# Kernel optimization log

Measured on AMD Instinct MI355X. Metric: run time of the kernel, lower is better.

The kernel has to match this reference:

```python
import jax, jax.numpy as jnp
import numpy as np

L, B, N, D, H = 2, 4, 2048, 1024, 16
DH = D // H
HID = 4 * D
EPS = 1e-5


def setup_inputs() -> dict:
    key = jax.random.key(0)
    ks = jax.random.split(key, 8)
    s = 0.02
    return {
        "tokens": jax.random.normal(ks[0], (B, N, D), jnp.float32),
        "ln1_g": jnp.ones((L, D), jnp.float32),
        "ln1_b": jnp.zeros((L, D), jnp.float32),
        "qkv_w": jax.random.normal(ks[1], (L, 3 * D, D), jnp.float32) * s,
        "qkv_b": jnp.zeros((L, 3 * D), jnp.float32),
        "out_w": jax.random.normal(ks[2], (L, D, D), jnp.float32) * s,
        "out_b": jnp.zeros((L, D), jnp.float32),
        "ln2_g": jnp.ones((L, D), jnp.float32),
        "ln2_b": jnp.zeros((L, D), jnp.float32),
        "fc1_w": jax.random.normal(ks[3], (L, HID, D), jnp.float32) * s,
        "fc1_b": jnp.zeros((L, HID), jnp.float32),
        "fc2_w": jax.random.normal(ks[4], (L, D, HID), jnp.float32) * s,
        "fc2_b": jnp.zeros((L, D), jnp.float32),
    }


def _layernorm(x, g, b):
    mu = jnp.mean(x, axis=-1, keepdims=True)
    var = jnp.mean(jnp.square(x - mu), axis=-1, keepdims=True)
    return (x - mu) * jax.lax.rsqrt(var + EPS) * g + b


def _mha(x, qkv_w, qkv_b, out_w, out_b):
    # nn.MultiheadAttention self-attention, batch_first=True
    qkv = x @ qkv_w.T + qkv_b                        # [B,N,3D]
    q, k, v = jnp.split(qkv, 3, axis=-1)
    q = q.reshape(B, N, H, DH)
    k = k.reshape(B, N, H, DH)
    v = v.reshape(B, N, H, DH)
    scores = jnp.einsum("bqhd,bkhd->bhqk", q, k) / np.sqrt(DH).astype(np.float32)
    attn = jax.nn.softmax(scores, axis=-1)
    o = jnp.einsum("bhqk,bkhd->bqhd", attn, v).reshape(B, N, D)
    return o @ out_w.T + out_b


def reference(tokens, ln1_g, ln1_b, qkv_w, qkv_b, out_w, out_b,
              ln2_g, ln2_b, fc1_w, fc1_b, fc2_w, fc2_b):
    x = tokens
    for i in range(L):
        # NOTE: the original reassigns tokens = norm1(tokens) before residual,
        # so the residual is taken on the NORMED tokens (faithful to source).
        x = _layernorm(x, ln1_g[i], ln1_b[i])
        x = x + _mha(x, qkv_w[i], qkv_b[i], out_w[i], out_b[i])
        x = _layernorm(x, ln2_g[i], ln2_b[i])
        h = jax.nn.gelu(x @ fc1_w[i].T + fc1_b[i], approximate=False)
        x = x + (h @ fc2_w[i].T + fc2_b[i])
    return x  # proj_out / norm_out are Identity since out_dim == dim
```

## Files before the change

### kernel.cpp

```cpp
#include <hip/hip_runtime.h>
#include <cstdint>
#include <cstddef>

typedef unsigned short u16;
typedef __attribute__((ext_vector_type(8))) short bf16x8;
typedef __attribute__((ext_vector_type(8))) u16  u16x8;
typedef __attribute__((ext_vector_type(4))) u16  u16x4;
typedef __attribute__((ext_vector_type(4))) float f32x4;
typedef __attribute__((ext_vector_type(16))) float f32x16;
typedef __attribute__((ext_vector_type(4))) unsigned u32x4;

static __device__ __forceinline__ u16 f2bf(float f) {
  unsigned u = __builtin_bit_cast(unsigned, f);
  u += 0x7fffu + ((u >> 16) & 1u);
  return (u16)(u >> 16);
}
static __device__ __forceinline__ float bf2f(u16 h) {
  return __builtin_bit_cast(float, (unsigned)h << 16);
}
static __device__ __forceinline__ unsigned cvtpk_bf16(float a, float b) {
  unsigned r;
  asm("v_cvt_pk_bf16_f32 %0, %1, %2" : "=v"(r) : "v"(a), "v"(b));
  return r;
}

static __device__ __forceinline__ void gload16(u16* lds, const u16* g) {
  __builtin_amdgcn_global_load_lds(
      (__attribute__((address_space(1))) unsigned int*)(void*)(g),
      (__attribute__((address_space(3))) unsigned int*)(lds), 16, 0, 0);
}

__global__ __launch_bounds__(256) void cast_f32_bf16(
    const float* __restrict__ s, u16* __restrict__ d, int n4) {
  int i = blockIdx.x * 256 + threadIdx.x;
  if (i < n4) {
    float4 v = ((const float4*)s)[i];
    u16x4 o;
    o[0] = f2bf(v.x); o[1] = f2bf(v.y); o[2] = f2bf(v.z); o[3] = f2bf(v.w);
    ((u16x4*)d)[i] = o;
  }
}

__global__ __launch_bounds__(256) void ln_kernel(
    const float* __restrict__ in, const float* __restrict__ g,
    const float* __restrict__ bb, float* __restrict__ outf,
    u16* __restrict__ outb) {
  const int row = blockIdx.x;
  const int t = threadIdx.x;
  const float4 v = ((const float4*)(in + (size_t)row * 1024))[t];
  float s  = v.x + v.y + v.z + v.w;
  float sq = v.x * v.x + v.y * v.y + v.z * v.z + v.w * v.w;
#pragma unroll
  for (int off = 32; off > 0; off >>= 1) {
    s  += __shfl_down(s, off);
    sq += __shfl_down(sq, off);
  }
  __shared__ float red[8];
  const int w = t >> 6;
  if ((t & 63) == 0) { red[w] = s; red[4 + w] = sq; }
  __syncthreads();
  const float ts  = red[0] + red[1] + red[2] + red[3];
  const float tsq = red[4] + red[5] + red[6] + red[7];
  const float mu = ts * (1.0f / 1024.0f);
  const float rv = rsqrtf(tsq * (1.0f / 1024.0f) - mu * mu + 1e-5f);
  const float4 gv = ((const float4*)g)[t];
  const float4 bv = ((const float4*)bb)[t];
  float4 y;
  y.x = (v.x - mu) * rv * gv.x + bv.x;
  y.y = (v.y - mu) * rv * gv.y + bv.y;
  y.z = (v.z - mu) * rv * gv.z + bv.z;
  y.w = (v.w - mu) * rv * gv.w + bv.w;
  ((float4*)(outf + (size_t)row * 1024))[t] = y;
  u16x4 ob;
  ob[0] = f2bf(y.x); ob[1] = f2bf(y.y); ob[2] = f2bf(y.z); ob[3] = f2bf(y.w);
  *(u16x4*)(outb + (size_t)row * 1024 + t * 4) = ob;
}

#define BM 128
#define BN 128
#define BK 32

template <int MODE>
__global__ __launch_bounds__(256) void gemm_bt(
    const u16* __restrict__ A, const u16* __restrict__ W,
    const float* __restrict__ bias, const float* __restrict__ res,
    u16* __restrict__ outb, float* __restrict__ outf, int Nn, int K) {
  __shared__ u16 As[BM * BK];
  __shared__ u16 Bs[BN * BK];
  const int t  = threadIdx.x;
  const int w  = t >> 6;
  const int ln = t & 63;
  const int lr = ln & 15;
  const int lg = ln >> 4;
  const int bm = blockIdx.x * BM;
  const int bn = blockIdx.y * BN;
  const int wm = (w >> 1) * 64;
  const int wn = (w & 1) * 64;

  f32x4 acc[4][4] = {};

  const int sr = t >> 2;
  const int sk = (t & 3) * 8;
  const u16* gA = A + (size_t)(bm + sr) * K + sk;
  const u16* gB = W + (size_t)(bn + sr) * K + sk;
  const int ldsOff = w * 512;

  const int kSteps = K >> 5;
  for (int kt = 0; kt < kSteps; ++kt) {
    __syncthreads();
    const u16* ga = gA + kt * BK;
    const u16* gb = gB + kt * BK;
    gload16(As + ldsOff,        ga);
    gload16(As + ldsOff + 2048, ga + (size_t)64 * K);
    gload16(Bs + ldsOff,        gb);
    gload16(Bs + ldsOff + 2048, gb + (size_t)64 * K);
    __syncthreads();

    bf16x8 af[4], bfr[4];
#pragma unroll
    for (int mi = 0; mi < 4; ++mi)
      af[mi] = *(const bf16x8*)(As + (wm + mi * 16 + lr) * BK + lg * 8);
#pragma unroll
    for (int ni = 0; ni < 4; ++ni)
      bfr[ni] = *(const bf16x8*)(Bs + (wn + ni * 16 + lr) * BK + lg * 8);
#pragma unroll
    for (int mi = 0; mi < 4; ++mi)
#pragma unroll
      for (int ni = 0; ni < 4; ++ni)
        acc[mi][ni] = __builtin_amdgcn_mfma_f32_16x16x32_bf16(
            af[mi], bfr[ni], acc[mi][ni], 0, 0, 0);
  }

#pragma unroll
  for (int ni = 0; ni < 4; ++ni) {
    const int col = bn + wn + ni * 16 + lr;
    const float bv = bias[col];
#pragma unroll
    for (int mi = 0; mi < 4; ++mi) {
      const int row0 = bm + wm + mi * 16 + lg * 4;
#pragma unroll
      for (int r = 0; r < 4; ++r) {
        float v = acc[mi][ni][r] + bv;
        const size_t idx = (size_t)(row0 + r) * Nn + col;
        if (MODE == 1) v = 0.5f * v * (1.0f + erff(v * 0.70710678118654752f));
        if (MODE == 2) outf[idx] = res[idx] + v;
        else           outb[idx] = f2bf(v);
      }
    }
  }
}

__global__ __launch_bounds__(256, 4) void attn_kernel(
    const u16* __restrict__ qkv, u16* __restrict__ o) {
  __shared__ u16 Ks[2 * 64 * 64];
  __shared__ u16 Vt[2 * 64 * 64];
  const int t   = threadIdx.x;
  const int w   = t >> 6;
  const int l   = t & 63;
  const int q31 = l & 31;
  const int h   = l >> 5;
  const int Lid = blockIdx.x;
  const int v_id = (Lid & 7) * 128 + (Lid >> 3);
  const int bh = v_id >> 4;
  const int b  = bh >> 4;
  const int hd = bh & 15;
  const int qb = (v_id & 15) * 128;
  const size_t baseRow = (size_t)b * 2048;
  const int hcol = hd * 64;

  bf16x8 qf[4];
  {
    const u16* qp = qkv + (baseRow + qb + w * 32 + q31) * 3072 + hcol + h * 8;
#pragma unroll
    for (int f = 0; f < 4; ++f) {
      u16x8 raw = *(const u16x8*)(qp + f * 16);
      bf16x8 q;
#pragma unroll
      for (int i = 0; i < 8; ++i)
        q[i] = (short)f2bf(bf2f(raw[i]) * 0.125f);
      qf[f] = q;
    }
  }

  f32x16 oacc[2] = {};
  float mrun = -3.0e38f, lrun = 0.0f;

  const int skey = t >> 3;
  const int dK   = 8 * ((t & 7) ^ (skey & 7));
  const int sd0  = (t & 7) * 8;

  {
    gload16(Ks + w * 512,        qkv + (baseRow + skey) * 3072      + 1024 + hcol + dK);
    gload16(Ks + 2048 + w * 512, qkv + (baseRow + 32 + skey) * 3072 + 1024 + hcol + dK);
    u16x8 va = *(const u16x8*)(qkv + (baseRow + skey) * 3072      + 2048 + hcol + sd0);
    u16x8 vb = *(const u16x8*)(qkv + (baseRow + 32 + skey) * 3072 + 2048 + hcol + sd0);
    char* VtB = (char*)Vt;
#pragma unroll
    for (int j = 0; j < 8; ++j) {
      const int sw = (j ^ (t & 7)) << 4;
      *(u16*)(VtB + ((((sd0 + j) * 128 + skey * 2)        ) ^ sw)) = va[j];
      *(u16*)(VtB + ((((sd0 + j) * 128 + (32 + skey) * 2) ) ^ sw)) = vb[j];
    }
  }
  __syncthreads();

  for (int kt = 0; kt < 32; ++kt) {
    char* const KsB = (char*)Ks + (kt & 1) * 8192;
    char* const VtB = (char*)Vt + (kt & 1) * 8192;
    u16* const KsN  = Ks + ((kt & 1) ^ 1) * 4096;
    char* const VtN = (char*)Vt + ((kt & 1) ^ 1) * 8192;

    u16x8 vva, vvb;
    const bool pf = (kt < 31);
    if (pf) {
      const size_t krow = baseRow + (size_t)(kt + 1) * 64;
      gload16(KsN + w * 512,        qkv + (krow + skey) * 3072      + 1024 + hcol + dK);
      gload16(KsN + 2048 + w * 512, qkv + (krow + 32 + skey) * 3072 + 1024 + hcol + dK);
      vva = *(const u16x8*)(qkv + (krow + skey) * 3072      + 2048 + hcol + sd0);
      vvb = *(const u16x8*)(qkv + (krow + 32 + skey) * 3072 + 2048 + hcol + sd0);
    }

    f32x16 s0 = {}, s1 = {};
#pragma unroll
    for (int f = 0; f < 4; ++f) {
      const int d0b = (f * 16 + h * 8) * 2;
      {
        const int row = q31;
        bf16x8 ka = *(const bf16x8*)(KsB + ((row * 128 + d0b) ^ ((row & 7) << 4)));
        s0 = __builtin_amdgcn_mfma_f32_32x32x16_bf16(ka, qf[f], s0, 0, 0, 0);
      }
      {
        const int row = 32 + q31;
        bf16x8 ka = *(const bf16x8*)(KsB + ((row * 128 + d0b) ^ ((row & 7) << 4)));
        s1 = __builtin_amdgcn_mfma_f32_32x32x16_bf16(ka, qf[f], s1, 0, 0, 0);
      }
    }

    float tm[16];
#pragma unroll
    for (int r = 0; r < 16; ++r) tm[r] = fmaxf(s0[r], s1[r]);
#pragma unroll
    for (int st = 8; st >= 1; st >>= 1)
#pragma unroll
      for (int r = 0; r < st; ++r) tm[r] = fmaxf(tm[r], tm[r + st]);
    const float mx = fmaxf(tm[0], __shfl_xor(tm[0], 32));
    const float mn = fmaxf(mrun, mx);
    const float al = __expf(mrun - mn);
    mrun = mn;
#pragma unroll
    for (int r = 0; r < 16; ++r) {
      s0[r] = __expf(s0[r] - mn);
      s1[r] = __expf(s1[r] - mn);
    }
    float tsum[16];
#pragma unroll
    for (int r = 0; r < 16; ++r) tsum[r] = s0[r] + s1[r];
#pragma unroll
    for (int st = 8; st >= 1; st >>= 1)
#pragma unroll
      for (int r = 0; r < st; ++r) tsum[r] += tsum[r + st];
    const float psum = tsum[0] + __shfl_xor(tsum[0], 32);
    lrun = lrun * al + psum;
#pragma unroll
    for (int r = 0; r < 16; ++r) { oacc[0][r] *= al; oacc[1][r] *= al; }

#pragma unroll
    for (int kw = 0; kw < 4; ++kw) {
      const int w1 = kw & 1;
      const f32x16 sv = (kw < 2) ? s0 : s1;
      const unsigned L0 = cvtpk_bf16(sv[8 * w1 + 0], sv[8 * w1 + 1]);
      const unsigned L1 = cvtpk_bf16(sv[8 * w1 + 2], sv[8 * w1 + 3]);
      const unsigned H0 = cvtpk_bf16(sv[8 * w1 + 4], sv[8 * w1 + 5]);
      const unsigned H1 = cvtpk_bf16(sv[8 * w1 + 6], sv[8 * w1 + 7]);
      const unsigned X0 = h ? L0 : H0;
      const unsigned X1 = h ? L1 : H1;
      const unsigned R0 = (unsigned)__shfl_xor((int)X0, 32);
      const unsigned R1 = (unsigned)__shfl_xor((int)X1, 32);
      u32x4 pw;
      pw[0] = h ? R0 : L0;
      pw[1] = h ? R1 : L1;
      pw[2] = h ? H0 : R0;
      pw[3] = h ? H1 : R1;
      const bf16x8 pb = __builtin_bit_cast(bf16x8, pw);
      const int k0b = (kw * 16 + h * 8) * 2;
#pragma unroll
      for (int dt = 0; dt < 2; ++dt) {
        const int d = dt * 32 + q31;
        bf16x8 va = *(const bf16x8*)(
            VtB + ((d * 128 + k0b) ^ ((((d & 7) ^ ((d >> 3) & 7))) << 4)));
        oacc[dt] = __builtin_amdgcn_mfma_f32_32x32x16_bf16(va, pb, oacc[dt], 0, 0, 0);
      }
    }

    if (pf) {
#pragma unroll
      for (int j = 0; j < 8; ++j) {
        const int sw = (j ^ (t & 7)) << 4;
        *(u16*)(VtN + ((((sd0 + j) * 128 + skey * 2)        ) ^ sw)) = vva[j];
        *(u16*)(VtN + ((((sd0 + j) * 128 + (32 + skey) * 2) ) ^ sw)) = vvb[j];
      }
    }
    __syncthreads();
  }

  const float inv = 1.0f / lrun;
  const size_t orow = baseRow + qb + w * 32 + q31;
#pragma unroll
  for (int dt = 0; dt < 2; ++dt)
#pragma unroll
    for (int g = 0; g < 4; ++g) {
      u16x4 ov;
#pragma unroll
      for (int j = 0; j < 4; ++j) ov[j] = f2bf(oacc[dt][g * 4 + j] * inv);
      *(u16x4*)(o + orow * 1024 + hcol + dt * 32 + g * 8 + h * 4) = ov;
    }
}

extern "C" void kernel_launch(void* const* d_in, const int* in_sizes, int n_in,
                              void* d_out, int out_size, void* d_ws,
                              size_t ws_size, hipStream_t stream) {
  const float* tokens = (const float*)d_in[0];
  const float* ln1_g  = (const float*)d_in[1];
  const float* ln1_b  = (const float*)d_in[2];
  const float* qkv_w  = (const float*)d_in[3];
  const float* qkv_b  = (const float*)d_in[4];
  const float* out_w  = (const float*)d_in[5];
  const float* out_b  = (const float*)d_in[6];
  const float* ln2_g  = (const float*)d_in[7];
  const float* ln2_b  = (const float*)d_in[8];
  const float* fc1_w  = (const float*)d_in[9];
  const float* fc1_b  = (const float*)d_in[10];
  const float* fc2_w  = (const float*)d_in[11];
  const float* fc2_b  = (const float*)d_in[12];
  float* xf = (float*)d_out;

  char* ws = (char*)d_ws;
  size_t off = 0;
  auto take = [&](size_t bytes) {
    char* p = ws + off;
    off += (bytes + 255) & ~(size_t)255;
    return p;
  };
  u16* xn    = (u16*)take((size_t)8192 * 1024 * 2);
  u16* big   = (u16*)take((size_t)8192 * 4096 * 2);
  u16* attnb = (u16*)take((size_t)8192 * 1024 * 2);
  u16* qkvw  = (u16*)take((size_t)2 * 3072 * 1024 * 2);
  u16* outw  = (u16*)take((size_t)2 * 1024 * 1024 * 2);
  u16* fc1w  = (u16*)take((size_t)2 * 4096 * 1024 * 2);
  u16* fc2w  = (u16*)take((size_t)2 * 1024 * 4096 * 2);
  u16* qkvb16 = big;
  u16* hb     = big;

  cast_f32_bf16<<<6144, 256, 0, stream>>>(qkv_w, qkvw, 2 * 3072 * 1024 / 4);
  cast_f32_bf16<<<2048, 256, 0, stream>>>(out_w, outw, 2 * 1024 * 1024 / 4);
  cast_f32_bf16<<<8192, 256, 0, stream>>>(fc1_w, fc1w, 2 * 4096 * 1024 / 4);
  cast_f32_bf16<<<8192, 256, 0, stream>>>(fc2_w, fc2w, 2 * 1024 * 4096 / 4);

  for (int i = 0; i < 2; ++i) {
    ln_kernel<<<8192, 256, 0, stream>>>(i == 0 ? tokens : xf,
                                        ln1_g + i * 1024, ln1_b + i * 1024, xf, xn);
    gemm_bt<0><<<dim3(64, 24), 256, 0, stream>>>(
        xn, qkvw + (size_t)i * 3072 * 1024, qkv_b + i * 3072, nullptr,
        qkvb16, nullptr, 3072, 1024);
    attn_kernel<<<1024, 256, 0, stream>>>(qkvb16, attnb);
    gemm_bt<2><<<dim3(64, 8), 256, 0, stream>>>(
        attnb, outw + (size_t)i * 1024 * 1024, out_b + i * 1024, xf,
        nullptr, xf, 1024, 1024);
    ln_kernel<<<8192, 256, 0, stream>>>(xf, ln2_g + i * 1024, ln2_b + i * 1024,
                                        xf, xn);
    gemm_bt<1><<<dim3(64, 32), 256, 0, stream>>>(
        xn, fc1w + (size_t)i * 4096 * 1024, fc1_b + i * 4096, nullptr,
        hb, nullptr, 4096, 1024);
    gemm_bt<2><<<dim3(64, 8), 256, 0, stream>>>(
        hb, fc2w + (size_t)i * 1024 * 4096, fc2_b + i * 1024, xf,
        nullptr, xf, 1024, 4096);
  }
}
```

Before: 1.001 ms.

## Double GEMM K-tile with XOR-swizzled LDS and use exp2 softmax in attention

```diff
diff --git a/kernel.cpp b/kernel.cpp
--- a/kernel.cpp
+++ b/kernel.cpp
@@ -78,7 +78,7 @@
 
 #define BM 128
 #define BN 128
-#define BK 32
+#define BK 64
 
 template <int MODE>
 __global__ __launch_bounds__(256) void gemm_bt(
@@ -99,36 +99,47 @@
 
   f32x4 acc[4][4] = {};
 
-  const int sr = t >> 2;
-  const int sk = (t & 3) * 8;
-  const u16* gA = A + (size_t)(bm + sr) * K + sk;
-  const u16* gB = W + (size_t)(bn + sr) * K + sk;
-  const int ldsOff = w * 512;
-
-  const int kSteps = K >> 5;
+  const int srow = t >> 3;
+  const int scol = 8 * ((t & 7) ^ (srow & 7));
+  const u16* gA = A + (size_t)(bm + srow) * K + scol;
+  const u16* gB = W + (size_t)(bn + srow) * K + scol;
+  const char* const AsB = (const char*)As;
+  const char* const BsB = (const char*)Bs;
+
+  const int kSteps = K >> 6;
   for (int kt = 0; kt < kSteps; ++kt) {
     __syncthreads();
     const u16* ga = gA + kt * BK;
     const u16* gb = gB + kt * BK;
-    gload16(As + ldsOff,        ga);
-    gload16(As + ldsOff + 2048, ga + (size_t)64 * K);
-    gload16(Bs + ldsOff,        gb);
-    gload16(Bs + ldsOff + 2048, gb + (size_t)64 * K);
+#pragma unroll
+    for (int c = 0; c < 4; ++c) {
+      gload16(As + c * 2048 + w * 512, ga + (size_t)(c * 32) * K);
+      gload16(Bs + c * 2048 + w * 512, gb + (size_t)(c * 32) * K);
+    }
     __syncthreads();
 
-    bf16x8 af[4], bfr[4];
-#pragma unroll
-    for (int mi = 0; mi < 4; ++mi)
-      af[mi] = *(const bf16x8*)(As + (wm + mi * 16 + lr) * BK + lg * 8);
-#pragma unroll
-    for (int ni = 0; ni < 4; ++ni)
-      bfr[ni] = *(const bf16x8*)(Bs + (wn + ni * 16 + lr) * BK + lg * 8);
-#pragma unroll
-    for (int mi = 0; mi < 4; ++mi)
-#pragma unroll
-      for (int ni = 0; ni < 4; ++ni)
-        acc[mi][ni] = __builtin_amdgcn_mfma_f32_16x16x32_bf16(
-            af[mi], bfr[ni], acc[mi][ni], 0, 0, 0);
+#pragma unroll
+    for (int kc = 0; kc < 2; ++kc) {
+      bf16x8 af[4], bfr[4];
+#pragma unroll
+      for (int mi = 0; mi < 4; ++mi) {
+        const int row = wm + mi * 16 + lr;
+        af[mi] = *(const bf16x8*)(
+            AsB + ((row * 128 + kc * 64 + lg * 16) ^ ((row & 7) << 4)));
+      }
+#pragma unroll
+      for (int ni = 0; ni < 4; ++ni) {
+        const int row = wn + ni * 16 + lr;
+        bfr[ni] = *(const bf16x8*)(
+            BsB + ((row * 128 + kc * 64 + lg * 16) ^ ((row & 7) << 4)));
+      }
+#pragma unroll
+      for (int mi = 0; mi < 4; ++mi)
+#pragma unroll
+        for (int ni = 0; ni < 4; ++ni)
+          acc[mi][ni] = __builtin_amdgcn_mfma_f32_16x16x32_bf16(
+              af[mi], bfr[ni], acc[mi][ni], 0, 0, 0);
+    }
   }
 
 #pragma unroll
@@ -171,13 +182,14 @@
   bf16x8 qf[4];
   {
     const u16* qp = qkv + (baseRow + qb + w * 32 + q31) * 3072 + hcol + h * 8;
+    const float qscale = 0.125f * 1.44269504088896f;
 #pragma unroll
     for (int f = 0; f < 4; ++f) {
       u16x8 raw = *(const u16x8*)(qp + f * 16);
       bf16x8 q;
 #pragma unroll
       for (int i = 0; i < 8; ++i)
-        q[i] = (short)f2bf(bf2f(raw[i]) * 0.125f);
+        q[i] = (short)f2bf(bf2f(raw[i]) * qscale);
       qf[f] = q;
     }
   }
@@ -245,12 +257,12 @@
       for (int r = 0; r < st; ++r) tm[r] = fmaxf(tm[r], tm[r + st]);
     const float mx = fmaxf(tm[0], __shfl_xor(tm[0], 32));
     const float mn = fmaxf(mrun, mx);
-    const float al = __expf(mrun - mn);
+    const float al = exp2f(mrun - mn);
     mrun = mn;
 #pragma unroll
     for (int r = 0; r < 16; ++r) {
-      s0[r] = __expf(s0[r] - mn);
-      s1[r] = __expf(s1[r] - mn);
+      s0[r] = exp2f(s0[r] - mn);
+      s1[r] = exp2f(s1[r] - mn);
     }
     float tsum[16];
 #pragma unroll
```

Result: no change. 1.006 ms (+0.5%).
